# Kernel tuning notes

Hardware: AMD Instinct MI355X
Metric: run time of the kernel (lower is better)

## Reference

```python
import jax, jax.numpy as jnp
import numpy as np
import math

B, S, D, H, N = 4, 2048, 1024, 8, 128  # batch, seq_len, d_model, n_heads, num_osc
ITERS = 10
DT = 0.1
PI = math.pi


def setup_inputs() -> dict:
    key = jax.random.key(0)
    ks = jax.random.split(key, 5)
    return {
        "x": jax.random.normal(ks[0], (B, S, D), jnp.float32),
        "mask": jnp.ones((B, S), jnp.int32),
        "W_phase": jax.random.normal(ks[1], (D, H * N), jnp.float32) / math.sqrt(D),
        "b_phase": jnp.zeros((H * N,), jnp.float32),
        "natural_freq": jax.random.normal(ks[2], (H, N), jnp.float32) * 0.1,
        "coupling": jnp.ones((H, 1, 1), jnp.float32),  # coupling_strength = 1.0
        "W_out": jax.random.normal(ks[3], (H * N, D), jnp.float32) / math.sqrt(H * N),
        "b_out": jnp.zeros((D,), jnp.float32),
    }


def reference(x, mask, W_phase, b_phase, natural_freq, coupling, W_out, b_out):
    # phases: [B, H, S, N]
    ph = (x @ W_phase + b_phase).reshape(B, S, H, N).transpose(0, 2, 1, 3)
    ph = jnp.tanh(ph) * PI
    m = mask.astype(ph.dtype)[:, None, :, None]  # [B,1,S,1] mask over j
    K = coupling.reshape(1, H, 1, 1)
    w = natural_freq.reshape(1, H, 1, N)

    def step(ph, _):
        s = jnp.sin(ph)
        c = jnp.cos(ph)
        # mean_j m_j * sin(theta_i - theta_j) = sin(th_i)*mean(m*cos) - cos(th_i)*mean(m*sin)
        ms = (m * s).mean(axis=2, keepdims=True)  # [B,H,1,N]
        mc = (m * c).mean(axis=2, keepdims=True)
        dtheta = w + K * (s * mc - c * ms)
        ph2 = jnp.mod(ph + DT * dtheta + PI, 2 * PI) - PI
        return ph2, None

    ph, _ = jax.lax.scan(step, ph, None, length=ITERS)
    # from_phase; dropout is identity in eval mode
    y = ph.transpose(0, 2, 1, 3).reshape(B, S, H * N) @ W_out + b_out
    return y
```

## Files before the change

### kernel.cpp

```cpp
#include <hip/hip_runtime.h>
#include <math.h>

#define S_ 2048
#define D_ 1024
#define HN_ 1024
#define B_ 4
#define M_ 8192
#define K1_ 3072
#define K3_ 1024
#define ITERS_ 10
#define DT_ 0.1f
#define PI_ 3.14159265358979323846f
#define TWOPI_ 6.28318530717958647692f
#define INV2PI_ 0.15915494309189533577f
#define SCALE_ 4096.0f
#define INVSC2_ (1.0f / 16777216.0f)

typedef __attribute__((ext_vector_type(8))) _Float16 f16x8;
typedef __attribute__((ext_vector_type(4))) float f32x4;

__device__ ushort g_xs [(size_t)M_ * K1_];
__device__ ushort g_WpT[(size_t)HN_ * K1_];
__device__ float  g_ph [(size_t)B_ * HN_ * S_];
__device__ ushort g_phh[(size_t)B_ * HN_ * S_];
__device__ ushort g_phT[(size_t)M_ * HN_];
__device__ ushort g_WoT[(size_t)D_ * HN_];

__device__ __forceinline__ ushort f2h(float f) {
    union { _Float16 h; ushort u; } v; v.h = (_Float16)f; return v.u;
}
__device__ __forceinline__ void split2s(float x, ushort& A, ushort& Bc) {
    const float xs = x * SCALE_;
    union { _Float16 h; ushort u; } va, vb;
    va.h = (_Float16)xs;
    const float r = xs - (float)va.h;
    vb.h = (_Float16)r;
    A = va.u; Bc = vb.u;
}
__device__ __forceinline__ void gload16(const void* g, void* l) {
    __builtin_amdgcn_global_load_lds(
        (const __attribute__((address_space(1))) void*)g,
        (__attribute__((address_space(3))) void*)l, 16, 0, 0);
}
__device__ __forceinline__ int pack2(ushort a, ushort b) {
    return (int)(unsigned)a | ((int)(unsigned)b << 16);
}

__global__ __launch_bounds__(256) void split_x(const float* __restrict__ X) {
    const int idx = blockIdx.x * 256 + threadIdx.x;
    const float4 v = ((const float4*)X)[idx];
    const int m  = idx >> 8;
    const int k4 = (idx & 255) * 4;
    ushort a[4], b[4];
    split2s(v.x, a[0], b[0]);
    split2s(v.y, a[1], b[1]);
    split2s(v.z, a[2], b[2]);
    split2s(v.w, a[3], b[3]);
    ushort* row = g_xs + (size_t)m * K1_ + k4;
    int2 oa; oa.x = pack2(a[0], a[1]); oa.y = pack2(a[2], a[3]);
    int2 ob; ob.x = pack2(b[0], b[1]); ob.y = pack2(b[2], b[3]);
    *(int2*)(row)        = oa;
    *(int2*)(row + 1024) = oa;
    *(int2*)(row + 2048) = ob;
}

__global__ __launch_bounds__(256) void splitT_Wp(const float* __restrict__ Wp) {
    __shared__ float t[64][68];
    const int k0 = blockIdx.x * 64;
    const int n0 = blockIdx.y * 64;
    const int r = threadIdx.x >> 2;
    const int c = (threadIdx.x & 3) * 16;
    const float* src = Wp + (size_t)(k0 + r) * HN_ + n0 + c;
    #pragma unroll
    for (int q = 0; q < 4; ++q)
        *(float4*)&t[r][c + 4 * q] = ((const float4*)src)[q];
    __syncthreads();
    ushort ha[16], hb[16];
    #pragma unroll
    for (int j = 0; j < 16; ++j)
        split2s(t[c + j][r], ha[j], hb[j]);
    int4 a0, a1, b0, b1;
    a0.x = pack2(ha[0], ha[1]);   a0.y = pack2(ha[2], ha[3]);
    a0.z = pack2(ha[4], ha[5]);   a0.w = pack2(ha[6], ha[7]);
    a1.x = pack2(ha[8], ha[9]);   a1.y = pack2(ha[10], ha[11]);
    a1.z = pack2(ha[12], ha[13]); a1.w = pack2(ha[14], ha[15]);
    b0.x = pack2(hb[0], hb[1]);   b0.y = pack2(hb[2], hb[3]);
    b0.z = pack2(hb[4], hb[5]);   b0.w = pack2(hb[6], hb[7]);
    b1.x = pack2(hb[8], hb[9]);   b1.y = pack2(hb[10], hb[11]);
    b1.z = pack2(hb[12], hb[13]); b1.w = pack2(hb[14], hb[15]);
    ushort* dst = g_WpT + (size_t)(n0 + r) * K1_ + k0 + c;
    *(int4*)(dst)            = a0; *(int4*)(dst + 8)        = a1;
    *(int4*)(dst + 1024)     = b0; *(int4*)(dst + 1032)     = b1;
    *(int4*)(dst + 2048)     = a0; *(int4*)(dst + 2056)     = a1;
}

__global__ __launch_bounds__(256) void castT_Wo(const float* __restrict__ Wo) {
    __shared__ float t[64][68];
    const int k0 = blockIdx.x * 64;
    const int n0 = blockIdx.y * 64;
    const int r = threadIdx.x >> 2;
    const int c = (threadIdx.x & 3) * 16;
    const float* src = Wo + (size_t)(k0 + r) * D_ + n0 + c;
    #pragma unroll
    for (int q = 0; q < 4; ++q)
        *(float4*)&t[r][c + 4 * q] = ((const float4*)src)[q];
    __syncthreads();
    ushort h[16];
    #pragma unroll
    for (int j = 0; j < 16; ++j) h[j] = f2h(t[c + j][r]);
    ushort* dst = g_WoT + (size_t)(n0 + r) * HN_ + k0 + c;
    int4 o0, o1;
    o0.x = pack2(h[0], h[1]);   o0.y = pack2(h[2], h[3]);
    o0.z = pack2(h[4], h[5]);   o0.w = pack2(h[6], h[7]);
    o1.x = pack2(h[8], h[9]);   o1.y = pack2(h[10], h[11]);
    o1.z = pack2(h[12], h[13]); o1.w = pack2(h[14], h[15]);
    *(int4*)dst = o0;
    *(int4*)(dst + 8) = o1;
}

template<int KDIM>
__device__ __forceinline__ void gemm_mainloop(const ushort* __restrict__ A,
                                              const ushort* __restrict__ Bm,
                                              ushort* As, ushort* Bs,
                                              int m0, int n0, int wid, int l,
                                              int wm, int wn,
                                              f32x4 (&acc)[4][4]) {
    const int ldrow = l >> 3;
    const int lcolB = (l & 7) * 16;
    for (int k0 = 0; k0 < KDIM; k0 += 64) {
        #pragma unroll
        for (int j = 0; j < 4; ++j) {
            const int row = wid * 32 + j * 8 + ldrow;
            const size_t gb = (size_t)k0 * 2 + lcolB;
            gload16((const char*)(A + (size_t)(m0 + row) * KDIM) + gb,
                    (char*)As + wid * 4096 + j * 1024);
            gload16((const char*)(Bm + (size_t)(n0 + row) * KDIM) + gb,
                    (char*)Bs + wid * 4096 + j * 1024);
        }
        __syncthreads();
        #pragma unroll
        for (int ks = 0; ks < 2; ++ks) {
            f16x8 af[4], bf[4];
            #pragma unroll
            for (int i = 0; i < 4; ++i)
                af[i] = *(const f16x8*)(As + (wm * 64 + i * 16 + (l & 15)) * 64 + ks * 32 + (l >> 4) * 8);
            #pragma unroll
            for (int i = 0; i < 4; ++i)
                bf[i] = *(const f16x8*)(Bs + (wn * 64 + i * 16 + (l & 15)) * 64 + ks * 32 + (l >> 4) * 8);
            #pragma unroll
            for (int i = 0; i < 4; ++i)
                #pragma unroll
                for (int jj = 0; jj < 4; ++jj)
                    acc[i][jj] = __builtin_amdgcn_mfma_f32_16x16x32_f16(af[i], bf[jj], acc[i][jj], 0, 0, 0);
        }
        __syncthreads();
    }
}

__global__ __launch_bounds__(256) void gemm1(const float* __restrict__ bias) {
    __shared__ ushort As[128 * 64];
    __shared__ ushort Bs[128 * 64];
    const int tid = threadIdx.x;
    const int wid = tid >> 6, l = tid & 63;
    const int bid = blockIdx.x;
    const int swz = (bid & 7) * 64 + (bid >> 3);
    const int m0 = (swz & 63) * 128, n0 = (swz >> 6) * 128;
    const int wm = wid >> 1, wn = wid & 1;

    f32x4 acc[4][4];
    #pragma unroll
    for (int i = 0; i < 4; ++i)
        #pragma unroll
        for (int j = 0; j < 4; ++j) acc[i][j] = (f32x4){0.f, 0.f, 0.f, 0.f};

    gemm_mainloop<K1_>(g_xs, g_WpT, As, Bs, m0, n0, wid, l, wm, wn, acc);

    const int r4 = (l >> 4) * 4;
    const int cn = l & 15;
    #pragma unroll
    for (int i = 0; i < 4; ++i) {
        const int mg = m0 + wm * 64 + i * 16 + r4;
        const int bidx = mg >> 11;
        const int sg = mg & 2047;
        #pragma unroll
        for (int jj = 0; jj < 4; ++jj) {
            const int ng = n0 + wn * 64 + jj * 16 + cn;
            const float bb = bias[ng];
            float4 o;
            o.x = PI_ * tanhf(fmaf(acc[i][jj][0], INVSC2_, bb));
            o.y = PI_ * tanhf(fmaf(acc[i][jj][1], INVSC2_, bb));
            o.z = PI_ * tanhf(fmaf(acc[i][jj][2], INVSC2_, bb));
            o.w = PI_ * tanhf(fmaf(acc[i][jj][3], INVSC2_, bb));
            *(float4*)(g_ph + ((size_t)bidx * HN_ + ng) * S_ + sg) = o;
        }
    }
}

__global__ __launch_bounds__(256) void gemm3(const float* __restrict__ bias,
                                             float* __restrict__ Y) {
    __shared__ ushort As[128 * 64];
    __shared__ ushort Bs[128 * 64];
    const int tid = threadIdx.x;
    const int wid = tid >> 6, l = tid & 63;
    const int bid = blockIdx.x;
    const int swz = (bid & 7) * 64 + (bid >> 3);
    const int m0 = (swz & 63) * 128, n0 = (swz >> 6) * 128;
    const int wm = wid >> 1, wn = wid & 1;

    f32x4 acc[4][4];
    #pragma unroll
    for (int i = 0; i < 4; ++i)
        #pragma unroll
        for (int j = 0; j < 4; ++j) acc[i][j] = (f32x4){0.f, 0.f, 0.f, 0.f};

    gemm_mainloop<K3_>(g_phT, g_WoT, As, Bs, m0, n0, wid, l, wm, wn, acc);

    const int r4 = (l >> 4) * 4;
    const int cn = l & 15;
    #pragma unroll
    for (int i = 0; i < 4; ++i) {
        const int mg = m0 + wm * 64 + i * 16 + r4;
        #pragma unroll
        for (int jj = 0; jj < 4; ++jj) {
            const int ng = n0 + wn * 64 + jj * 16 + cn;
            const float bb = bias[ng];
            #pragma unroll
            for (int r = 0; r < 4; ++r)
                Y[(size_t)(mg + r) * D_ + ng] = acc[i][jj][r] + bb;
        }
    }
}

__global__ __launch_bounds__(256) void kuramoto(const int* __restrict__ mask,
                                                const float* __restrict__ natf,
                                                const float* __restrict__ coup) {
    const int wave = blockIdx.x * 4 + (threadIdx.x >> 6);
    const int lane = threadIdx.x & 63;
    const int b = wave >> 10;
    const int hn = wave & 1023;
    const int h = hn >> 7;

    const float wf = natf[hn];
    const float K = coup[h];

    const float* base = g_ph + ((size_t)b * HN_ + hn) * S_;

    float ph[32];
    #pragma unroll
    for (int i = 0; i < 8; ++i) {
        float4 v = *(const float4*)(base + i * 256 + lane * 4);
        ph[4 * i + 0] = v.x; ph[4 * i + 1] = v.y;
        ph[4 * i + 2] = v.z; ph[4 * i + 3] = v.w;
    }

    const int* mb = mask + b * S_;
    unsigned mbits = 0;
    #pragma unroll
    for (int i = 0; i < 8; ++i) {
        int4 mv = *(const int4*)(mb + i * 256 + lane * 4);
        mbits |= (mv.x != 0 ? 1u : 0u) << (4 * i + 0);
        mbits |= (mv.y != 0 ? 1u : 0u) << (4 * i + 1);
        mbits |= (mv.z != 0 ? 1u : 0u) << (4 * i + 2);
        mbits |= (mv.w != 0 ? 1u : 0u) << (4 * i + 3);
    }

    for (int it = 0; it < ITERS_; ++it) {
        float s[32], c[32];
        float ls = 0.f, lc = 0.f;
        #pragma unroll
        for (int i = 0; i < 32; ++i) {
            s[i] = __sinf(ph[i]);
            c[i] = __cosf(ph[i]);
            const float mf = (float)((mbits >> i) & 1u);
            ls = fmaf(mf, s[i], ls);
            lc = fmaf(mf, c[i], lc);
        }
        #pragma unroll
        for (int off = 32; off; off >>= 1) {
            ls += __shfl_xor(ls, off);
            lc += __shfl_xor(lc, off);
        }
        const float ms = ls * (1.f / 2048.f);
        const float mc = lc * (1.f / 2048.f);
        #pragma unroll
        for (int i = 0; i < 32; ++i) {
            const float dth = fmaf(K, fmaf(s[i], mc, -c[i] * ms), wf);
            float t = fmaf(DT_, dth, ph[i]) + PI_;
            t -= TWOPI_ * floorf(t * INV2PI_);
            ph[i] = t - PI_;
        }
    }

    ushort* ob = g_phh + ((size_t)b * HN_ + hn) * S_;
    #pragma unroll
    for (int i = 0; i < 8; ++i) {
        ushort4 o;
        o.x = f2h(ph[4 * i + 0]); o.y = f2h(ph[4 * i + 1]);
        o.z = f2h(ph[4 * i + 2]); o.w = f2h(ph[4 * i + 3]);
        *(ushort4*)(ob + i * 256 + lane * 4) = o;
    }
}

__global__ __launch_bounds__(256) void transpose_ph() {
    __shared__ ushort t[64][72];
    const int b = blockIdx.z;
    const int h0 = blockIdx.y * 64;
    const int s0 = blockIdx.x * 64;
    const int r = threadIdx.x >> 2;
    const int c = (threadIdx.x & 3) * 16;
    const ushort* src = g_phh + ((size_t)b * HN_ + h0 + r) * S_ + s0 + c;
    *(int4*)&t[r][c] = *(const int4*)src;
    *(int4*)&t[r][c + 8] = *(const int4*)(src + 8);
    __syncthreads();
    ushort o[16];
    #pragma unroll
    for (int j = 0; j < 16; ++j) o[j] = t[c + j][r];
    ushort* dst = g_phT + ((size_t)(b * S_ + s0 + r)) * HN_ + h0 + c;
    int4 o0, o1;
    o0.x = pack2(o[0], o[1]);   o0.y = pack2(o[2], o[3]);
    o0.z = pack2(o[4], o[5]);   o0.w = pack2(o[6], o[7]);
    o1.x = pack2(o[8], o[9]);   o1.y = pack2(o[10], o[11]);
    o1.z = pack2(o[12], o[13]); o1.w = pack2(o[14], o[15]);
    *(int4*)dst = o0;
    *(int4*)(dst + 8) = o1;
}

extern "C" void kernel_launch(void* const* d_in, const int* in_sizes, int n_in,
                              void* d_out, int out_size, void* d_ws, size_t ws_size,
                              hipStream_t stream) {
    const float* x    = (const float*)d_in[0];
    const int*   mask = (const int*)d_in[1];
    const float* Wp   = (const float*)d_in[2];
    const float* bp   = (const float*)d_in[3];
    const float* natf = (const float*)d_in[4];
    const float* coup = (const float*)d_in[5];
    const float* Wo   = (const float*)d_in[6];
    const float* bo   = (const float*)d_in[7];
    float* y = (float*)d_out;

    split_x  <<<dim3(8192),        256, 0, stream>>>(x);
    splitT_Wp<<<dim3(16, 16),      256, 0, stream>>>(Wp);
    castT_Wo <<<dim3(16, 16),      256, 0, stream>>>(Wo);
    gemm1    <<<dim3(512),         256, 0, stream>>>(bp);
    kuramoto <<<dim3(1024),        256, 0, stream>>>(mask, natf, coup);
    transpose_ph<<<dim3(32, 16, 4), 256, 0, stream>>>();
    gemm3    <<<dim3(512),         256, 0, stream>>>(bo, y);
}
```

Before: 195.2 us.

## Triple-buffer GEMM mainloop with swizzled LDS and 256x128 tiles on 8 waves

Rewrites the shared GEMM mainloop to prefetch two K-tiles ahead into a three-stage LDS ring, using explicit vmcnt waits and a single barrier per tile instead of two. LDS addresses are XOR-swizzled to avoid bank conflicts, and MFMA issue is wrapped in raised wave priority. Both GEMMs move to 512-thread blocks computing 256x128 tiles, which halves the grid and raises per-block reuse. The cost is 144 KB of LDS per block, which limits occupancy to one block per CU, plus extra hand-tuned synchronisation to get right.

```diff
diff --git a/kernel.cpp b/kernel.cpp
--- a/kernel.cpp
+++ b/kernel.cpp
@@ -121,50 +121,77 @@
 template<int KDIM>
 __device__ __forceinline__ void gemm_mainloop(const ushort* __restrict__ A,
                                               const ushort* __restrict__ Bm,
-                                              ushort* As, ushort* Bs,
+                                              ushort* lds,
                                               int m0, int n0, int wid, int l,
                                               int wm, int wn,
                                               f32x4 (&acc)[4][4]) {
-    const int ldrow = l >> 3;
-    const int lcolB = (l & 7) * 16;
-    for (int k0 = 0; k0 < KDIM; k0 += 64) {
-        #pragma unroll
-        for (int j = 0; j < 4; ++j) {
-            const int row = wid * 32 + j * 8 + ldrow;
-            const size_t gb = (size_t)k0 * 2 + lcolB;
-            gload16((const char*)(A + (size_t)(m0 + row) * KDIM) + gb,
-                    (char*)As + wid * 4096 + j * 1024);
-            gload16((const char*)(Bm + (size_t)(n0 + row) * KDIM) + gb,
-                    (char*)Bs + wid * 4096 + j * 1024);
-        }
-        __syncthreads();
+    constexpr int NT = KDIM / 64;
+    const int r8   = l >> 3;
+    const int swzo = ((l & 7) * 16) ^ (r8 << 4);
+
+    #define STAGE(T, BUF) do {                                                   \
+        const size_t gb_ = (size_t)(T) * 128 + swzo;                             \
+        char* ab_ = (char*)lds + (BUF) * 49152;                                  \
+        _Pragma("unroll")                                                        \
+        for (int j_ = 0; j_ < 4; ++j_) {                                         \
+            const int c_ = wid * 4 + j_;                                         \
+            gload16((const char*)(A + (size_t)(m0 + c_ * 8 + r8) * KDIM) + gb_,  \
+                    ab_ + c_ * 1024);                                            \
+        }                                                                        \
+        _Pragma("unroll")                                                        \
+        for (int j_ = 0; j_ < 2; ++j_) {                                         \
+            const int c_ = wid * 2 + j_;                                         \
+            gload16((const char*)(Bm + (size_t)(n0 + c_ * 8 + r8) * KDIM) + gb_, \
+                    ab_ + 32768 + c_ * 1024);                                    \
+        }                                                                        \
+    } while (0)
+
+    STAGE(0, 0);
+    STAGE(1, 1);
+
+    for (int t = 0; t < NT; ++t) {
+        if (t < NT - 1) asm volatile("s_waitcnt vmcnt(6)" ::: "memory");
+        else            asm volatile("s_waitcnt vmcnt(0)" ::: "memory");
+        __builtin_amdgcn_sched_barrier(0);
+        __builtin_amdgcn_s_barrier();
+        __builtin_amdgcn_sched_barrier(0);
+        if (t + 2 < NT) STAGE(t + 2, (t + 2) % 3);
+
+        const char* ab = (const char*)lds + (t % 3) * 49152;
+        const char* bb = ab + 32768;
         #pragma unroll
         for (int ks = 0; ks < 2; ++ks) {
+            const int kb = ks * 64 + (l >> 4) * 16;
             f16x8 af[4], bf[4];
             #pragma unroll
-            for (int i = 0; i < 4; ++i)
-                af[i] = *(const f16x8*)(As + (wm * 64 + i * 16 + (l & 15)) * 64 + ks * 32 + (l >> 4) * 8);
+            for (int i = 0; i < 4; ++i) {
+                const int r = wm * 64 + i * 16 + (l & 15);
+                af[i] = *(const f16x8*)(ab + r * 128 + (kb ^ ((r & 7) << 4)));
+            }
             #pragma unroll
-            for (int i = 0; i < 4; ++i)
-                bf[i] = *(const f16x8*)(Bs + (wn * 64 + i * 16 + (l & 15)) * 64 + ks * 32 + (l >> 4) * 8);
+            for (int i = 0; i < 4; ++i) {
+                const int r = wn * 64 + i * 16 + (l & 15);
+                bf[i] = *(const f16x8*)(bb + r * 128 + (kb ^ ((r & 7) << 4)));
+            }
+            __builtin_amdgcn_s_setprio(1);
             #pragma unroll
             for (int i = 0; i < 4; ++i)
                 #pragma unroll
                 for (int jj = 0; jj < 4; ++jj)
                     acc[i][jj] = __builtin_amdgcn_mfma_f32_16x16x32_f16(af[i], bf[jj], acc[i][jj], 0, 0, 0);
-        }
-        __syncthreads();
-    }
-}
-
-__global__ __launch_bounds__(256) void gemm1(const float* __restrict__ bias) {
-    __shared__ ushort As[128 * 64];
-    __shared__ ushort Bs[128 * 64];
+            __builtin_amdgcn_s_setprio(0);
+        }
+    }
+    #undef STAGE
+}
+
+__global__ __launch_bounds__(512) void gemm1(const float* __restrict__ bias) {
+    __shared__ ushort lds[3 * 24576];
     const int tid = threadIdx.x;
     const int wid = tid >> 6, l = tid & 63;
     const int bid = blockIdx.x;
-    const int swz = (bid & 7) * 64 + (bid >> 3);
-    const int m0 = (swz & 63) * 128, n0 = (swz >> 6) * 128;
+    const int swz = (bid & 7) * 32 + (bid >> 3);
+    const int m0 = (swz & 31) * 256, n0 = (swz >> 5) * 128;
     const int wm = wid >> 1, wn = wid & 1;
 
     f32x4 acc[4][4];
@@ -173,7 +200,7 @@
         #pragma unroll
         for (int j = 0; j < 4; ++j) acc[i][j] = (f32x4){0.f, 0.f, 0.f, 0.f};
 
-    gemm_mainloop<K1_>(g_xs, g_WpT, As, Bs, m0, n0, wid, l, wm, wn, acc);
+    gemm_mainloop<K1_>(g_xs, g_WpT, lds, m0, n0, wid, l, wm, wn, acc);
 
     const int r4 = (l >> 4) * 4;
     const int cn = l & 15;
@@ -196,15 +223,14 @@
     }
 }
 
-__global__ __launch_bounds__(256) void gemm3(const float* __restrict__ bias,
+__global__ __launch_bounds__(512) void gemm3(const float* __restrict__ bias,
                                              float* __restrict__ Y) {
-    __shared__ ushort As[128 * 64];
-    __shared__ ushort Bs[128 * 64];
+    __shared__ ushort lds[3 * 24576];
     const int tid = threadIdx.x;
     const int wid = tid >> 6, l = tid & 63;
     const int bid = blockIdx.x;
-    const int swz = (bid & 7) * 64 + (bid >> 3);
-    const int m0 = (swz & 63) * 128, n0 = (swz >> 6) * 128;
+    const int swz = (bid & 7) * 32 + (bid >> 3);
+    const int m0 = (swz & 31) * 256, n0 = (swz >> 5) * 128;
     const int wm = wid >> 1, wn = wid & 1;
 
     f32x4 acc[4][4];
@@ -213,7 +239,7 @@
         #pragma unroll
         for (int j = 0; j < 4; ++j) acc[i][j] = (f32x4){0.f, 0.f, 0.f, 0.f};
 
-    gemm_mainloop<K3_>(g_phT, g_WoT, As, Bs, m0, n0, wid, l, wm, wn, acc);
+    gemm_mainloop<K3_>(g_phT, g_WoT, lds, m0, n0, wid, l, wm, wn, acc);
 
     const int r4 = (l >> 4) * 4;
     const int cn = l & 15;
@@ -338,11 +364,11 @@
     const float* bo   = (const float*)d_in[7];
     float* y = (float*)d_out;
 
-    split_x  <<<dim3(8192),        256, 0, stream>>>(x);
-    splitT_Wp<<<dim3(16, 16),      256, 0, stream>>>(Wp);
-    castT_Wo <<<dim3(16, 16),      256, 0, stream>>>(Wo);
-    gemm1    <<<dim3(512),         256, 0, stream>>>(bp);
-    kuramoto <<<dim3(1024),        256, 0, stream>>>(mask, natf, coup);
+    split_x  <<<dim3(8192),         256, 0, stream>>>(x);
+    splitT_Wp<<<dim3(16, 16),       256, 0, stream>>>(Wp);
+    castT_Wo <<<dim3(16, 16),       256, 0, stream>>>(Wo);
+    gemm1    <<<dim3(256),          512, 0, stream>>>(bp);
+    kuramoto <<<dim3(1024),         256, 0, stream>>>(mask, natf, coup);
     transpose_ph<<<dim3(32, 16, 4), 256, 0, stream>>>();
-    gemm3    <<<dim3(512),         256, 0, stream>>>(bo, y);
-}
+    gemm3    <<<dim3(256),          512, 0, stream>>>(bo, y);
+}
```

Measured after the change: 174.0 us. -10.9%, faster.
